# Kernel optimization log

Hardware: AMD Instinct MI355X
Metric: run time of the kernel (lower is better)

## Reference

```python
import jax, jax.numpy as jnp
import numpy as np

N_BATCH = 128   # C: number of PWL channels / generator batch
N_PTS = 32768   # N: samples per channel
K_PWL = 20      # breakpoints per piecewise-linear function
LATENT = 8
HID = 8
EPS = 1e-7


def _mlp(z, W1, b1, W2, b2):
    # torch mlp: Linear -> Tanh -> Linear -> Tanh
    h = jnp.tanh(z @ W1 + b1)
    return jnp.tanh(h @ W2 + b2)


def _normalize01(a):
    # per-row min/max normalization, a: [C, N]
    a = a - a.min(axis=1, keepdims=True)
    return a / a.max(axis=1, keepdims=True)


def _calibrate1d(x, xp, yp):
    # x: [N, C], xp/yp: [C, K]
    N, C = x.shape
    K = xp.shape[1]
    bp = jnp.concatenate([x[:, :, None], jnp.broadcast_to(xp[None], (N, C, K))], axis=2)  # [N,C,K+1]
    order = jnp.argsort(bp, axis=2)                       # [N,C,K+1]
    sorted_bp = jnp.take_along_axis(bp, order, axis=2)
    x_idx = jnp.argmin(order, axis=2)                     # rank of x among breakpoints
    cand = x_idx - 1
    start_idx = jnp.where(x_idx == 0, 1, jnp.where(x_idx == K, K - 2, cand))
    end_idx = jnp.where(start_idx == cand, start_idx + 2, start_idx + 1)
    start_x = jnp.take_along_axis(sorted_bp, start_idx[..., None], axis=2)[..., 0]
    end_x = jnp.take_along_axis(sorted_bp, end_idx[..., None], axis=2)[..., 0]
    start_idx2 = jnp.where(x_idx == 0, 0, jnp.where(x_idx == K, K - 2, cand))
    yp_e = jnp.broadcast_to(yp[None], (N, C, K))
    start_y = jnp.take_along_axis(yp_e, start_idx2[..., None], axis=2)[..., 0]
    end_y = jnp.take_along_axis(yp_e, (start_idx2 + 1)[..., None], axis=2)[..., 0]
    return start_y + (x - start_x) * (end_y - start_y) / (end_x - start_x + EPS)


def setup_inputs() -> dict:
    key = jax.random.key(0)
    ks = jax.random.split(key, 16)
    s = 0.5
    f32 = jnp.float32
    return {
        "zf": jax.random.normal(ks[0], (N_BATCH, LATENT), f32),
        "zx": jax.random.normal(ks[1], (N_BATCH, N_PTS, LATENT), f32),
        "ze": jax.random.normal(ks[2], (N_BATCH, N_PTS, LATENT), f32),
        "Wx1": jax.random.normal(ks[3], (LATENT, HID), f32) * s,
        "bx1": jax.random.normal(ks[4], (HID,), f32) * s,
        "Wx2": jax.random.normal(ks[5], (HID, 1), f32) * s,
        "bx2": jax.random.normal(ks[6], (1,), f32) * s,
        "We1": jax.random.normal(ks[7], (LATENT, HID), f32) * s,
        "be1": jax.random.normal(ks[8], (HID,), f32) * s,
        "We2": jax.random.normal(ks[9], (HID, 1), f32) * s,
        "be2": jax.random.normal(ks[10], (1,), f32) * s,
        "Wf1": jax.random.normal(ks[11], (LATENT, HID), f32) * s,
        "bf1": jax.random.normal(ks[12], (HID,), f32) * s,
        "Wf2": jax.random.normal(ks[13], (HID, K_PWL), f32) * s,
        "bf2": jax.random.normal(ks[14], (K_PWL,), f32) * s,
        "directions": jax.random.randint(ks[15], (N_BATCH,), 0, 2) > 0,
    }


def reference(zf, zx, ze, Wx1, bx1, Wx2, bx2, We1, be1, We2, be2, Wf1, bf1, Wf2, bf2, directions):
    # gen_f: random ascending/descending monotone PWL per channel
    pts = _mlp(zf, Wf1, bf1, Wf2, bf2)                        # [C, K]
    asc = jnp.sort(pts, axis=1)
    yp = jnp.where(directions[:, None], asc, asc[:, ::-1])    # [C, K]
    xp = jnp.broadcast_to(jnp.linspace(0.0, 1.0, K_PWL, dtype=pts.dtype)[None, :], yp.shape)
    # forward_x: cause variable, per-channel normalized to [0,1]
    x = _mlp(zx, Wx1, bx1, Wx2, bx2)[..., 0]                  # [C, N]
    x = _normalize01(x).T                                     # [N, C]
    # forward_e: standardized noise (global mean / unbiased std)
    e = _mlp(ze, We1, be1, We2, be2)[..., 0].T                # [N, C]
    e = (e - e.mean()) / e.std(ddof=1)
    # forward_y
    y = _calibrate1d(x, xp, yp) + 0.1 * e                     # [N, C]
    return y
```

## Files before the change

### kernel.cpp

```cpp
#include <hip/hip_runtime.h>

#define C_CH  128
#define NP    32768
#define K_PWL 20
#define LAT   8
#define HID   8
#define SLOTS 32
#define PTS   4

__device__ __forceinline__ float fast_tanh(float x) {
    float e = __expf(2.0f * x);
    return fmaf(-2.0f, __builtin_amdgcn_rcpf(e + 1.0f), 1.0f);
}

__device__ __forceinline__ unsigned fenc(float f) {
    unsigned u = __float_as_uint(f);
    return (u & 0x80000000u) ? ~u : (u | 0x80000000u);
}
__device__ __forceinline__ float fdec(unsigned e) {
    unsigned u = (e & 0x80000000u) ? (e ^ 0x80000000u) : ~e;
    return __uint_as_float(u);
}

__global__ void prep(const float* __restrict__ zf,
                     const float* __restrict__ Wf1, const float* __restrict__ bf1,
                     const float* __restrict__ Wf2, const float* __restrict__ bf2,
                     const unsigned char* __restrict__ dirs_raw,
                     float* __restrict__ ypw,
                     unsigned* cminE, unsigned* cmaxE, double* sums) {
    int t = threadIdx.x;
    if (t < C_CH) { cminE[t] = 0xFFFFFFFFu; cmaxE[t] = 0u; }
    if (t < 2 * SLOTS) sums[t] = 0.0;

    __shared__ int is_i32;
    if (t == 0) {
        const int* di = (const int*)dirs_raw;
        int ok = 1;
        for (int i = 0; i < 32; i++) { int v = di[i]; if (v != 0 && v != 1) ok = 0; }
        is_i32 = ok;
    }
    __syncthreads();
    if (t >= C_CH) return;
    int c = t;

    float z[LAT];
    #pragma unroll
    for (int l = 0; l < LAT; l++) z[l] = zf[c * LAT + l];
    float h[HID];
    #pragma unroll
    for (int j = 0; j < HID; j++) {
        float a = bf1[j];
        #pragma unroll
        for (int l = 0; l < LAT; l++) a = fmaf(z[l], Wf1[l * HID + j], a);
        h[j] = fast_tanh(a);
    }
    float p[K_PWL];
    #pragma unroll
    for (int k = 0; k < K_PWL; k++) {
        float a = bf2[k];
        #pragma unroll
        for (int j = 0; j < HID; j++) a = fmaf(h[j], Wf2[j * K_PWL + k], a);
        p[k] = fast_tanh(a);
    }
    for (int i = 1; i < K_PWL; i++) {
        float key = p[i];
        int j = i - 1;
        while (j >= 0 && p[j] > key) { p[j + 1] = p[j]; j--; }
        p[j + 1] = key;
    }
    int dir = is_i32 ? (((const int*)dirs_raw)[c] != 0) : (dirs_raw[c] != 0);
    for (int k = 0; k < K_PWL; k++)
        ypw[c * K_PWL + k] = dir ? p[k] : p[K_PWL - 1 - k];
}

__global__ __launch_bounds__(256)
void pass1(const float* __restrict__ zx, const float* __restrict__ ze,
           const float* __restrict__ Wx1, const float* __restrict__ bx1,
           const float* __restrict__ Wx2, const float* __restrict__ bx2,
           const float* __restrict__ We1, const float* __restrict__ be1,
           const float* __restrict__ We2, const float* __restrict__ be2,
           float* __restrict__ xraw, float* __restrict__ eraw,
           unsigned* __restrict__ cminE, unsigned* __restrict__ cmaxE,
           double* __restrict__ sums) {
    __shared__ float sw[162];
    int t = threadIdx.x;
    if (t < 64)       sw[t] = Wx1[t];
    else if (t < 72)  sw[t] = bx1[t - 64];
    else if (t < 80)  sw[t] = Wx2[t - 72];
    else if (t == 80) sw[80] = bx2[0];
    else if (t < 145) sw[t] = We1[t - 81];
    else if (t < 153) sw[t] = be1[t - 145];
    else if (t < 161) sw[t] = We2[t - 153];
    else if (t == 161) sw[161] = be2[0];
    __syncthreads();

    int c = blockIdx.y;
    int n0 = blockIdx.x * (256 * PTS) + t;
    size_t row = (size_t)c * NP;
    const float4* zx4 = (const float4*)(zx + row * LAT);
    const float4* ze4 = (const float4*)(ze + row * LAT);

    float4 ax[PTS][2], ae[PTS][2];
    #pragma unroll
    for (int k = 0; k < PTS; k++) {
        int n = n0 + k * 256;
        ax[k][0] = zx4[2 * n];  ax[k][1] = zx4[2 * n + 1];
        ae[k][0] = ze4[2 * n];  ae[k][1] = ze4[2 * n + 1];
    }

    float xv[PTS], ev[PTS];
    #pragma unroll
    for (int k = 0; k < PTS; k++) {
        float acc = sw[80];
        #pragma unroll
        for (int j = 0; j < HID; j++) {
            float hh = sw[64 + j];
            hh = fmaf(ax[k][0].x, sw[0 * 8 + j], hh);
            hh = fmaf(ax[k][0].y, sw[1 * 8 + j], hh);
            hh = fmaf(ax[k][0].z, sw[2 * 8 + j], hh);
            hh = fmaf(ax[k][0].w, sw[3 * 8 + j], hh);
            hh = fmaf(ax[k][1].x, sw[4 * 8 + j], hh);
            hh = fmaf(ax[k][1].y, sw[5 * 8 + j], hh);
            hh = fmaf(ax[k][1].z, sw[6 * 8 + j], hh);
            hh = fmaf(ax[k][1].w, sw[7 * 8 + j], hh);
            acc = fmaf(fast_tanh(hh), sw[72 + j], acc);
        }
        xv[k] = fast_tanh(acc);
    }
    #pragma unroll
    for (int k = 0; k < PTS; k++) {
        float acc = sw[161];
        #pragma unroll
        for (int j = 0; j < HID; j++) {
            float hh = sw[145 + j];
            hh = fmaf(ae[k][0].x, sw[81 + 0 * 8 + j], hh);
            hh = fmaf(ae[k][0].y, sw[81 + 1 * 8 + j], hh);
            hh = fmaf(ae[k][0].z, sw[81 + 2 * 8 + j], hh);
            hh = fmaf(ae[k][0].w, sw[81 + 3 * 8 + j], hh);
            hh = fmaf(ae[k][1].x, sw[81 + 4 * 8 + j], hh);
            hh = fmaf(ae[k][1].y, sw[81 + 5 * 8 + j], hh);
            hh = fmaf(ae[k][1].z, sw[81 + 6 * 8 + j], hh);
            hh = fmaf(ae[k][1].w, sw[81 + 7 * 8 + j], hh);
            acc = fmaf(fast_tanh(hh), sw[153 + j], acc);
        }
        ev[k] = fast_tanh(acc);
    }

    float mn = xv[0], mx = xv[0], s = 0.f, s2 = 0.f;
    #pragma unroll
    for (int k = 0; k < PTS; k++) {
        xraw[row + n0 + k * 256] = xv[k];
        eraw[row + n0 + k * 256] = ev[k];
        mn = fminf(mn, xv[k]); mx = fmaxf(mx, xv[k]);
        s += ev[k]; s2 += ev[k] * ev[k];
    }

    #pragma unroll
    for (int o = 32; o > 0; o >>= 1) {
        mn = fminf(mn, __shfl_down(mn, o));
        mx = fmaxf(mx, __shfl_down(mx, o));
        s += __shfl_down(s, o);
        s2 += __shfl_down(s2, o);
    }
    __shared__ float rmn[4], rmx[4], rs[4], rs2[4];
    int wave = t >> 6, lane = t & 63;
    if (lane == 0) { rmn[wave] = mn; rmx[wave] = mx; rs[wave] = s; rs2[wave] = s2; }
    __syncthreads();
    if (t == 0) {
        for (int w = 1; w < 4; w++) {
            mn = fminf(mn, rmn[w]); mx = fmaxf(mx, rmx[w]);
            s += rs[w]; s2 += rs2[w];
        }
        atomicMin(&cminE[c], fenc(mn));
        atomicMax(&cmaxE[c], fenc(mx));
        int slot = (blockIdx.x + blockIdx.y) & (SLOTS - 1);
        atomicAdd(&sums[2 * slot], (double)s);
        atomicAdd(&sums[2 * slot + 1], (double)s2);
    }
}

__global__ __launch_bounds__(256)
void pass2(const float* __restrict__ xraw, const float* __restrict__ eraw,
           const float* __restrict__ ypw,
           const unsigned* __restrict__ cminE, const unsigned* __restrict__ cmaxE,
           const double* __restrict__ sums,
           float* __restrict__ out) {
    __shared__ float ytile[C_CH * 33];
    __shared__ float syp[C_CH * K_PWL];
    __shared__ float smin[C_CH], sinv[C_CH];
    __shared__ float sstat[2];

    int t = threadIdx.x;
    for (int i = t; i < C_CH * K_PWL; i += 256) syp[i] = ypw[i];
    if (t < C_CH) {
        float mn = fdec(cminE[t]);
        float mx = fdec(cmaxE[t]);
        smin[t] = mn;
        sinv[t] = __builtin_amdgcn_rcpf(mx - mn);
    }
    if (t == 0) {
        double s = 0.0, s2 = 0.0;
        for (int i = 0; i < SLOTS; i++) { s += sums[2 * i]; s2 += sums[2 * i + 1]; }
        double M = (double)C_CH * NP;
        double mean = s / M;
        double var = (s2 - s * s / M) / (M - 1.0);
        sstat[0] = (float)mean;
        sstat[1] = (float)(0.1 / sqrt(var));
    }
    __syncthreads();

    const float INV_DENOM = 1.0f / (1.0f / 19.0f + 1e-7f);
    float mean = sstat[0], escale = sstat[1];
    int n0 = blockIdx.x * 32;

    #pragma unroll
    for (int i = 0; i < 16; i++) {
        int idx = i * 256 + t;
        int c = idx >> 5;
        int j = idx & 31;
        size_t g = (size_t)c * NP + (n0 + j);
        float x = xraw[g];
        float e = eraw[g];
        float xn = (x - smin[c]) * sinv[c];
        int seg = (int)floorf(xn * 19.0f);
        seg = max(0, min(18, seg));
        float y0 = syp[c * K_PWL + seg];
        float y1 = syp[c * K_PWL + seg + 1];
        float y = fmaf((xn - (float)seg * (1.0f / 19.0f)) * INV_DENOM, y1 - y0, y0);
        y = fmaf(e - mean, escale, y);
        ytile[c * 33 + j] = y;
    }
    __syncthreads();
    #pragma unroll
    for (int i = 0; i < 16; i++) {
        int idx = i * 256 + t;
        int j = idx >> 7;
        int c = idx & 127;
        out[(size_t)(n0 + j) * C_CH + c] = ytile[c * 33 + j];
    }
}

extern "C" void kernel_launch(void* const* d_in, const int* in_sizes, int n_in,
                              void* d_out, int out_size, void* d_ws, size_t ws_size,
                              hipStream_t stream) {
    const float* zf  = (const float*)d_in[0];
    const float* zx  = (const float*)d_in[1];
    const float* ze  = (const float*)d_in[2];
    const float* Wx1 = (const float*)d_in[3];
    const float* bx1 = (const float*)d_in[4];
    const float* Wx2 = (const float*)d_in[5];
    const float* bx2 = (const float*)d_in[6];
    const float* We1 = (const float*)d_in[7];
    const float* be1 = (const float*)d_in[8];
    const float* We2 = (const float*)d_in[9];
    const float* be2 = (const float*)d_in[10];
    const float* Wf1 = (const float*)d_in[11];
    const float* bf1 = (const float*)d_in[12];
    const float* Wf2 = (const float*)d_in[13];
    const float* bf2 = (const float*)d_in[14];
    const unsigned char* dirs = (const unsigned char*)d_in[15];

    float* xraw = (float*)d_ws;
    float* eraw = xraw + (size_t)C_CH * NP;
    float* ypw  = eraw + (size_t)C_CH * NP;
    unsigned* cminE = (unsigned*)(ypw + C_CH * K_PWL);
    unsigned* cmaxE = cminE + C_CH;
    double* sums = (double*)(cmaxE + C_CH);

    hipLaunchKernelGGL(prep, dim3(1), dim3(256), 0, stream,
                       zf, Wf1, bf1, Wf2, bf2, dirs, ypw, cminE, cmaxE, sums);
    hipLaunchKernelGGL(pass1, dim3(NP / (256 * PTS), C_CH), dim3(256), 0, stream,
                       zx, ze, Wx1, bx1, Wx2, bx2, We1, be1, We2, be2,
                       xraw, eraw, cminE, cmaxE, sums);
    hipLaunchKernelGGL(pass2, dim3(NP / 32), dim3(256), 0, stream,
                       xraw, eraw, ypw, cminE, cmaxE, sums, (float*)d_out);
}
```

Measured before the change: 344.1 us.

## Fuse prep, pass1 and pass2 into one cooperative kernel with grid syncs

Result: no change. 342.0 us (-0.6%).

```diff
diff --git a/kernel.cpp b/kernel.cpp
--- a/kernel.cpp
+++ b/kernel.cpp
@@ -1,4 +1,7 @@
 #include <hip/hip_runtime.h>
+#include <hip/hip_cooperative_groups.h>
+
+namespace cg = cooperative_groups;
 
 #define C_CH  128
 #define NP    32768
@@ -7,6 +10,8 @@
 #define HID   8
 #define SLOTS 32
 #define PTS   4
+#define NBLK  512
+#define TN    64
 
 __device__ __forceinline__ float fast_tanh(float x) {
     float e = __expf(2.0f * x);
@@ -20,6 +25,239 @@
 __device__ __forceinline__ float fdec(unsigned e) {
     unsigned u = (e & 0x80000000u) ? (e ^ 0x80000000u) : ~e;
     return __uint_as_float(u);
+}
+
+__device__ __forceinline__ float mlp_eval(const float* W, float4 r0, float4 r1) {
+    float acc = W[80];
+    #pragma unroll
+    for (int j = 0; j < HID; j++) {
+        float hh = W[64 + j];
+        hh = fmaf(r0.x, W[0 * 8 + j], hh);
+        hh = fmaf(r0.y, W[1 * 8 + j], hh);
+        hh = fmaf(r0.z, W[2 * 8 + j], hh);
+        hh = fmaf(r0.w, W[3 * 8 + j], hh);
+        hh = fmaf(r1.x, W[4 * 8 + j], hh);
+        hh = fmaf(r1.y, W[5 * 8 + j], hh);
+        hh = fmaf(r1.z, W[6 * 8 + j], hh);
+        hh = fmaf(r1.w, W[7 * 8 + j], hh);
+        acc = fmaf(fast_tanh(hh), W[72 + j], acc);
+    }
+    return fast_tanh(acc);
+}
+
+__global__ __launch_bounds__(256, 2)
+void fused(const float* __restrict__ zf, const float* __restrict__ zx,
+           const float* __restrict__ ze,
+           const float* __restrict__ Wx1, const float* __restrict__ bx1,
+           const float* __restrict__ Wx2, const float* __restrict__ bx2,
+           const float* __restrict__ We1, const float* __restrict__ be1,
+           const float* __restrict__ We2, const float* __restrict__ be2,
+           const float* __restrict__ Wf1, const float* __restrict__ bf1,
+           const float* __restrict__ Wf2, const float* __restrict__ bf2,
+           const unsigned char* __restrict__ dirs_raw,
+           float* __restrict__ out,
+           double* __restrict__ psum,
+           float* __restrict__ pmin,
+           float* __restrict__ pmax,
+           float* __restrict__ gmm,
+           float* __restrict__ gstat) {
+    __shared__ float sx[C_CH * (TN + 1)];
+    __shared__ float se[C_CH * TN];
+    __shared__ float syp[C_CH * K_PWL];
+    __shared__ float sw[162];
+    __shared__ float smin[C_CH], sinv[C_CH];
+    __shared__ float sstat2[2];
+    __shared__ float rf[8];
+    __shared__ double rsd[8];
+    __shared__ int is_i32;
+
+    int t = threadIdx.x;
+    int b = blockIdx.x;
+    int w = t >> 6, lane = t & 63;
+
+    if (t < 64)        sw[t] = Wx1[t];
+    else if (t < 72)   sw[t] = bx1[t - 64];
+    else if (t < 80)   sw[t] = Wx2[t - 72];
+    else if (t == 80)  sw[80] = bx2[0];
+    else if (t < 145)  sw[t] = We1[t - 81];
+    else if (t < 153)  sw[t] = be1[t - 145];
+    else if (t < 161)  sw[t] = We2[t - 153];
+    else if (t == 161) sw[161] = be2[0];
+    if (t == 192) {
+        const int* di = (const int*)dirs_raw;
+        int ok = 1;
+        for (int i = 0; i < 32; i++) { int v = di[i]; if (v != 0 && v != 1) ok = 0; }
+        is_i32 = ok;
+    }
+    __syncthreads();
+
+    int n0 = b * TN;
+    const float4* zx4 = (const float4*)zx + ((size_t)w * NP + n0 + lane) * 2;
+    const float4* ze4 = (const float4*)ze + ((size_t)w * NP + n0 + lane) * 2;
+    const size_t STEP = (size_t)4 * NP * 2;
+
+    float ssum = 0.f, ss2 = 0.f;
+    float4 A0 = zx4[0], A1 = zx4[1], AE0 = ze4[0], AE1 = ze4[1];
+    float4 B0 = zx4[STEP], B1 = zx4[STEP + 1], BE0 = ze4[STEP], BE1 = ze4[STEP + 1];
+    #pragma unroll 2
+    for (int i = 0; i < 32; i++) {
+        float4 C0, C1, CE0, CE1;
+        if (i + 2 < 32) {
+            size_t o = (size_t)(i + 2) * STEP;
+            C0 = zx4[o]; C1 = zx4[o + 1]; CE0 = ze4[o]; CE1 = ze4[o + 1];
+        } else { C0 = B0; C1 = B1; CE0 = BE0; CE1 = BE1; }
+        float xv = mlp_eval(sw, A0, A1);
+        float ev = mlp_eval(sw + 81, AE0, AE1);
+        int idx = i * 256 + t;
+        sx[idx + (idx >> 6)] = xv;
+        se[idx] = ev;
+        ssum += ev;
+        ss2 = fmaf(ev, ev, ss2);
+        A0 = B0; A1 = B1; AE0 = BE0; AE1 = BE1;
+        B0 = C0; B1 = C1; BE0 = CE0; BE1 = CE1;
+    }
+
+    #pragma unroll
+    for (int o = 32; o > 0; o >>= 1) {
+        ssum += __shfl_down(ssum, o);
+        ss2  += __shfl_down(ss2, o);
+    }
+    if (lane == 0) { rf[w] = ssum; rf[4 + w] = ss2; }
+    __syncthreads();
+
+    if (t < C_CH) {
+        float mn = 3.0e38f, mx = -3.0e38f;
+        int base = t * (TN + 1);
+        #pragma unroll 8
+        for (int j = 0; j < TN; j++) {
+            float v = sx[base + j];
+            mn = fminf(mn, v); mx = fmaxf(mx, v);
+        }
+        pmin[b * C_CH + t] = mn;
+        pmax[b * C_CH + t] = mx;
+        if (t == 0) {
+            double S  = (double)rf[0] + (double)rf[1] + (double)rf[2] + (double)rf[3];
+            double S2 = (double)rf[4] + (double)rf[5] + (double)rf[6] + (double)rf[7];
+            psum[2 * b] = S; psum[2 * b + 1] = S2;
+        }
+    } else {
+        int c = t - 128;
+        float z[LAT];
+        #pragma unroll
+        for (int l = 0; l < LAT; l++) z[l] = zf[c * LAT + l];
+        float h[HID];
+        #pragma unroll
+        for (int j = 0; j < HID; j++) {
+            float a = bf1[j];
+            #pragma unroll
+            for (int l = 0; l < LAT; l++) a = fmaf(z[l], Wf1[l * HID + j], a);
+            h[j] = fast_tanh(a);
+        }
+        float p[K_PWL];
+        #pragma unroll
+        for (int k = 0; k < K_PWL; k++) {
+            float a = bf2[k];
+            #pragma unroll
+            for (int j = 0; j < HID; j++) a = fmaf(h[j], Wf2[j * K_PWL + k], a);
+            p[k] = fast_tanh(a);
+        }
+        #pragma unroll
+        for (int ph = 0; ph < K_PWL; ph++) {
+            #pragma unroll
+            for (int k = (ph & 1); k + 1 < K_PWL; k += 2) {
+                float lo = fminf(p[k], p[k + 1]);
+                float hi = fmaxf(p[k], p[k + 1]);
+                p[k] = lo; p[k + 1] = hi;
+            }
+        }
+        int dir = is_i32 ? (((const int*)dirs_raw)[c] != 0) : (dirs_raw[c] != 0);
+        #pragma unroll
+        for (int k = 0; k < K_PWL; k++)
+            syp[c * K_PWL + k] = dir ? p[k] : p[K_PWL - 1 - k];
+    }
+
+    __threadfence();
+    cg::grid_group grid = cg::this_grid();
+    grid.sync();
+
+    if (b < C_CH) {
+        const volatile float* vmin = pmin;
+        const volatile float* vmax = pmax;
+        float mn = fminf(vmin[(size_t)t * C_CH + b], vmin[(size_t)(t + 256) * C_CH + b]);
+        float mx = fmaxf(vmax[(size_t)t * C_CH + b], vmax[(size_t)(t + 256) * C_CH + b]);
+        #pragma unroll
+        for (int o = 32; o > 0; o >>= 1) {
+            mn = fminf(mn, __shfl_down(mn, o));
+            mx = fmaxf(mx, __shfl_down(mx, o));
+        }
+        if (lane == 0) { rf[w] = mn; rf[4 + w] = mx; }
+        __syncthreads();
+        if (t == 0) {
+            mn = fminf(fminf(rf[0], rf[1]), fminf(rf[2], rf[3]));
+            mx = fmaxf(fmaxf(rf[4], rf[5]), fmaxf(rf[6], rf[7]));
+            gmm[b] = mn; gmm[C_CH + b] = mx;
+        }
+    } else if (b == C_CH) {
+        const volatile double* vs = psum;
+        double S  = vs[2 * t]     + vs[2 * (t + 256)];
+        double S2 = vs[2 * t + 1] + vs[2 * (t + 256) + 1];
+        #pragma unroll
+        for (int o = 32; o > 0; o >>= 1) {
+            S  += __shfl_down(S, o);
+            S2 += __shfl_down(S2, o);
+        }
+        if (lane == 0) { rsd[w] = S; rsd[4 + w] = S2; }
+        __syncthreads();
+        if (t == 0) {
+            S  = rsd[0] + rsd[1] + rsd[2] + rsd[3];
+            S2 = rsd[4] + rsd[5] + rsd[6] + rsd[7];
+            double M = (double)C_CH * NP;
+            double mean = S / M;
+            double var = (S2 - S * S / M) / (M - 1.0);
+            gstat[0] = (float)mean;
+            gstat[1] = (float)(0.1 / sqrt(var));
+        }
+    }
+    __threadfence();
+    grid.sync();
+
+    if (t < C_CH) {
+        const volatile float* g = gmm;
+        float mn = g[t], mx = g[C_CH + t];
+        smin[t] = mn;
+        sinv[t] = __builtin_amdgcn_rcpf(mx - mn);
+    }
+    if (t == 0) {
+        const volatile float* gs = gstat;
+        sstat2[0] = gs[0]; sstat2[1] = gs[1];
+    }
+    __syncthreads();
+
+    const float INV_DENOM = 1.0f / (1.0f / 19.0f + 1e-7f);
+    float mean = sstat2[0], escale = sstat2[1];
+    #pragma unroll 4
+    for (int i = 0; i < 32; i++) {
+        int idx = i * 256 + t;
+        int c = idx >> 6;
+        float x = sx[idx + c];
+        float e = se[idx];
+        float xn = (x - smin[c]) * sinv[c];
+        int seg = (int)floorf(xn * 19.0f);
+        seg = max(0, min(18, seg));
+        float y0 = syp[c * K_PWL + seg];
+        float y1 = syp[c * K_PWL + seg + 1];
+        float y = fmaf((xn - (float)seg * (1.0f / 19.0f)) * INV_DENOM, y1 - y0, y0);
+        y = fmaf(e - mean, escale, y);
+        sx[idx + c] = y;
+    }
+    __syncthreads();
+    #pragma unroll 4
+    for (int ii = 0; ii < 32; ii++) {
+        int idx2 = ii * 256 + t;
+        int c = idx2 & 127;
+        int j = idx2 >> 7;
+        out[(size_t)(n0 + j) * C_CH + c] = sx[c * (TN + 1) + j];
+    }
 }
 
 __global__ void prep(const float* __restrict__ zf,
@@ -110,41 +348,9 @@
 
     float xv[PTS], ev[PTS];
     #pragma unroll
-    for (int k = 0; k < PTS; k++) {
-        float acc = sw[80];
-        #pragma unroll
-        for (int j = 0; j < HID; j++) {
-            float hh = sw[64 + j];
-            hh = fmaf(ax[k][0].x, sw[0 * 8 + j], hh);
-            hh = fmaf(ax[k][0].y, sw[1 * 8 + j], hh);
-            hh = fmaf(ax[k][0].z, sw[2 * 8 + j], hh);
-            hh = fmaf(ax[k][0].w, sw[3 * 8 + j], hh);
-            hh = fmaf(ax[k][1].x, sw[4 * 8 + j], hh);
-            hh = fmaf(ax[k][1].y, sw[5 * 8 + j], hh);
-            hh = fmaf(ax[k][1].z, sw[6 * 8 + j], hh);
-            hh = fmaf(ax[k][1].w, sw[7 * 8 + j], hh);
-            acc = fmaf(fast_tanh(hh), sw[72 + j], acc);
-        }
-        xv[k] = fast_tanh(acc);
-    }
-    #pragma unroll
-    for (int k = 0; k < PTS; k++) {
-        float acc = sw[161];
-        #pragma unroll
-        for (int j = 0; j < HID; j++) {
-            float hh = sw[145 + j];
-            hh = fmaf(ae[k][0].x, sw[81 + 0 * 8 + j], hh);
-            hh = fmaf(ae[k][0].y, sw[81 + 1 * 8 + j], hh);
-            hh = fmaf(ae[k][0].z, sw[81 + 2 * 8 + j], hh);
-            hh = fmaf(ae[k][0].w, sw[81 + 3 * 8 + j], hh);
-            hh = fmaf(ae[k][1].x, sw[81 + 4 * 8 + j], hh);
-            hh = fmaf(ae[k][1].y, sw[81 + 5 * 8 + j], hh);
-            hh = fmaf(ae[k][1].z, sw[81 + 6 * 8 + j], hh);
-            hh = fmaf(ae[k][1].w, sw[81 + 7 * 8 + j], hh);
-            acc = fmaf(fast_tanh(hh), sw[153 + j], acc);
-        }
-        ev[k] = fast_tanh(acc);
-    }
+    for (int k = 0; k < PTS; k++) xv[k] = mlp_eval(sw, ax[k][0], ax[k][1]);
+    #pragma unroll
+    for (int k = 0; k < PTS; k++) ev[k] = mlp_eval(sw + 81, ae[k][0], ae[k][1]);
 
     float mn = xv[0], mx = xv[0], s = 0.f, s2 = 0.f;
     #pragma unroll
@@ -259,6 +465,38 @@
     const float* Wf2 = (const float*)d_in[13];
     const float* bf2 = (const float*)d_in[14];
     const unsigned char* dirs = (const unsigned char*)d_in[15];
+    float* outp = (float*)d_out;
+
+    static int mode = -1;
+    if (mode < 0) {
+        int dev = 0, coop = 0, nb = 0;
+        hipGetDevice(&dev);
+        hipDeviceGetAttribute(&coop, hipDeviceAttributeCooperativeLaunch, dev);
+        hipError_t oe = hipOccupancyMaxActiveBlocksPerMultiprocessor(
+            &nb, reinterpret_cast<const void*>(fused), 256, 0);
+        mode = (coop && oe == hipSuccess && nb >= 2) ? 1 : 0;
+    }
+
+    if (mode == 1) {
+        double* psum  = (double*)d_ws;
+        float*  pmin  = (float*)(psum + 2 * NBLK);
+        float*  pmax  = pmin + NBLK * C_CH;
+        float*  gmm   = pmax + NBLK * C_CH;
+        float*  gstat = gmm + 2 * C_CH;
+        void* args[] = {
+            (void*)&zf,  (void*)&zx,  (void*)&ze,
+            (void*)&Wx1, (void*)&bx1, (void*)&Wx2, (void*)&bx2,
+            (void*)&We1, (void*)&be1, (void*)&We2, (void*)&be2,
+            (void*)&Wf1, (void*)&bf1, (void*)&Wf2, (void*)&bf2,
+            (void*)&dirs, (void*)&outp,
+            (void*)&psum, (void*)&pmin, (void*)&pmax, (void*)&gmm, (void*)&gstat
+        };
+        hipError_t le = hipLaunchCooperativeKernel(
+            reinterpret_cast<const void*>(fused), dim3(NBLK), dim3(256),
+            args, 0, stream);
+        if (le == hipSuccess) return;
+        mode = 0;
+    }
 
     float* xraw = (float*)d_ws;
     float* eraw = xraw + (size_t)C_CH * NP;
@@ -273,5 +511,5 @@
                        zx, ze, Wx1, bx1, Wx2, bx2, We1, be1, We2, be2,
                        xraw, eraw, cminE, cmaxE, sums);
     hipLaunchKernelGGL(pass2, dim3(NP / 32), dim3(256), 0, stream,
-                       xraw, eraw, ypw, cminE, cmaxE, sums, (float*)d_out);
-}
+                       xraw, eraw, ypw, cminE, cmaxE, sums, outp);
+}
```

## Store pass1 intermediates in pass2 tile layout and halve points per thread

Applied to the files above, without the earlier changes.

After: 416.6 us. 1.21x slower.

```diff
diff --git a/kernel.cpp b/kernel.cpp
--- a/kernel.cpp
+++ b/kernel.cpp
@@ -6,7 +6,7 @@
 #define LAT   8
 #define HID   8
 #define SLOTS 32
-#define PTS   4
+#define P1PTS 2
 
 __device__ __forceinline__ float fast_tanh(float x) {
     float e = __expf(2.0f * x);
@@ -20,6 +20,24 @@
 __device__ __forceinline__ float fdec(unsigned e) {
     unsigned u = (e & 0x80000000u) ? (e ^ 0x80000000u) : ~e;
     return __uint_as_float(u);
+}
+
+__device__ __forceinline__ float mlp_eval(const float* W, float4 r0, float4 r1) {
+    float acc = W[80];
+    #pragma unroll
+    for (int j = 0; j < HID; j++) {
+        float hh = W[64 + j];
+        hh = fmaf(r0.x, W[0 * 8 + j], hh);
+        hh = fmaf(r0.y, W[1 * 8 + j], hh);
+        hh = fmaf(r0.z, W[2 * 8 + j], hh);
+        hh = fmaf(r0.w, W[3 * 8 + j], hh);
+        hh = fmaf(r1.x, W[4 * 8 + j], hh);
+        hh = fmaf(r1.y, W[5 * 8 + j], hh);
+        hh = fmaf(r1.z, W[6 * 8 + j], hh);
+        hh = fmaf(r1.w, W[7 * 8 + j], hh);
+        acc = fmaf(fast_tanh(hh), W[72 + j], acc);
+    }
+    return fast_tanh(acc);
 }
 
 __global__ void prep(const float* __restrict__ zf,
@@ -73,15 +91,15 @@
         ypw[c * K_PWL + k] = dir ? p[k] : p[K_PWL - 1 - k];
 }
 
-__global__ __launch_bounds__(256)
-void pass1(const float* __restrict__ zx, const float* __restrict__ ze,
-           const float* __restrict__ Wx1, const float* __restrict__ bx1,
-           const float* __restrict__ Wx2, const float* __restrict__ bx2,
-           const float* __restrict__ We1, const float* __restrict__ be1,
-           const float* __restrict__ We2, const float* __restrict__ be2,
-           float* __restrict__ xraw, float* __restrict__ eraw,
-           unsigned* __restrict__ cminE, unsigned* __restrict__ cmaxE,
-           double* __restrict__ sums) {
+__global__ __launch_bounds__(256, 8)
+void pass1t(const float* __restrict__ zx, const float* __restrict__ ze,
+            const float* __restrict__ Wx1, const float* __restrict__ bx1,
+            const float* __restrict__ Wx2, const float* __restrict__ bx2,
+            const float* __restrict__ We1, const float* __restrict__ be1,
+            const float* __restrict__ We2, const float* __restrict__ be2,
+            float* __restrict__ xtile, float* __restrict__ etile,
+            unsigned* __restrict__ cminE, unsigned* __restrict__ cmaxE,
+            double* __restrict__ sums) {
     __shared__ float sw[162];
     int t = threadIdx.x;
     if (t < 64)       sw[t] = Wx1[t];
@@ -95,62 +113,33 @@
     __syncthreads();
 
     int c = blockIdx.y;
-    int n0 = blockIdx.x * (256 * PTS) + t;
+    int n0 = blockIdx.x * (256 * P1PTS) + t;
     size_t row = (size_t)c * NP;
     const float4* zx4 = (const float4*)(zx + row * LAT);
     const float4* ze4 = (const float4*)(ze + row * LAT);
 
-    float4 ax[PTS][2], ae[PTS][2];
-    #pragma unroll
-    for (int k = 0; k < PTS; k++) {
+    float4 ax[P1PTS][2], ae[P1PTS][2];
+    #pragma unroll
+    for (int k = 0; k < P1PTS; k++) {
         int n = n0 + k * 256;
         ax[k][0] = zx4[2 * n];  ax[k][1] = zx4[2 * n + 1];
         ae[k][0] = ze4[2 * n];  ae[k][1] = ze4[2 * n + 1];
     }
 
-    float xv[PTS], ev[PTS];
-    #pragma unroll
-    for (int k = 0; k < PTS; k++) {
-        float acc = sw[80];
-        #pragma unroll
-        for (int j = 0; j < HID; j++) {
-            float hh = sw[64 + j];
-            hh = fmaf(ax[k][0].x, sw[0 * 8 + j], hh);
-            hh = fmaf(ax[k][0].y, sw[1 * 8 + j], hh);
-            hh = fmaf(ax[k][0].z, sw[2 * 8 + j], hh);
-            hh = fmaf(ax[k][0].w, sw[3 * 8 + j], hh);
-            hh = fmaf(ax[k][1].x, sw[4 * 8 + j], hh);
-            hh = fmaf(ax[k][1].y, sw[5 * 8 + j], hh);
-            hh = fmaf(ax[k][1].z, sw[6 * 8 + j], hh);
-            hh = fmaf(ax[k][1].w, sw[7 * 8 + j], hh);
-            acc = fmaf(fast_tanh(hh), sw[72 + j], acc);
-        }
-        xv[k] = fast_tanh(acc);
-    }
-    #pragma unroll
-    for (int k = 0; k < PTS; k++) {
-        float acc = sw[161];
-        #pragma unroll
-        for (int j = 0; j < HID; j++) {
-            float hh = sw[145 + j];
-            hh = fmaf(ae[k][0].x, sw[81 + 0 * 8 + j], hh);
-            hh = fmaf(ae[k][0].y, sw[81 + 1 * 8 + j], hh);
-            hh = fmaf(ae[k][0].z, sw[81 + 2 * 8 + j], hh);
-            hh = fmaf(ae[k][0].w, sw[81 + 3 * 8 + j], hh);
-            hh = fmaf(ae[k][1].x, sw[81 + 4 * 8 + j], hh);
-            hh = fmaf(ae[k][1].y, sw[81 + 5 * 8 + j], hh);
-            hh = fmaf(ae[k][1].z, sw[81 + 6 * 8 + j], hh);
-            hh = fmaf(ae[k][1].w, sw[81 + 7 * 8 + j], hh);
-            acc = fmaf(fast_tanh(hh), sw[153 + j], acc);
-        }
-        ev[k] = fast_tanh(acc);
-    }
+    float xv[P1PTS], ev[P1PTS];
+    #pragma unroll
+    for (int k = 0; k < P1PTS; k++) xv[k] = mlp_eval(sw, ax[k][0], ax[k][1]);
+    #pragma unroll
+    for (int k = 0; k < P1PTS; k++) ev[k] = mlp_eval(sw + 81, ae[k][0], ae[k][1]);
 
     float mn = xv[0], mx = xv[0], s = 0.f, s2 = 0.f;
-    #pragma unroll
-    for (int k = 0; k < PTS; k++) {
-        xraw[row + n0 + k * 256] = xv[k];
-        eraw[row + n0 + k * 256] = ev[k];
+    int cbase = c * 32;
+    #pragma unroll
+    for (int k = 0; k < P1PTS; k++) {
+        int n = n0 + k * 256;
+        int addr = (n >> 5) * (C_CH * 32) + cbase + (n & 31);
+        xtile[addr] = xv[k];
+        etile[addr] = ev[k];
         mn = fminf(mn, xv[k]); mx = fmaxf(mx, xv[k]);
         s += ev[k]; s2 += ev[k] * ev[k];
     }
@@ -180,11 +169,11 @@
 }
 
 __global__ __launch_bounds__(256)
-void pass2(const float* __restrict__ xraw, const float* __restrict__ eraw,
-           const float* __restrict__ ypw,
-           const unsigned* __restrict__ cminE, const unsigned* __restrict__ cmaxE,
-           const double* __restrict__ sums,
-           float* __restrict__ out) {
+void pass2t(const float* __restrict__ xtile, const float* __restrict__ etile,
+            const float* __restrict__ ypw,
+            const unsigned* __restrict__ cminE, const unsigned* __restrict__ cmaxE,
+            const double* __restrict__ sums,
+            float* __restrict__ out) {
     __shared__ float ytile[C_CH * 33];
     __shared__ float syp[C_CH * K_PWL];
     __shared__ float smin[C_CH], sinv[C_CH];
@@ -211,6 +200,7 @@
 
     const float INV_DENOM = 1.0f / (1.0f / 19.0f + 1e-7f);
     float mean = sstat[0], escale = sstat[1];
+    size_t tbase = (size_t)blockIdx.x * (C_CH * 32);
     int n0 = blockIdx.x * 32;
 
     #pragma unroll
@@ -218,9 +208,8 @@
         int idx = i * 256 + t;
         int c = idx >> 5;
         int j = idx & 31;
-        size_t g = (size_t)c * NP + (n0 + j);
-        float x = xraw[g];
-        float e = eraw[g];
+        float x = xtile[tbase + idx];
+        float e = etile[tbase + idx];
         float xn = (x - smin[c]) * sinv[c];
         int seg = (int)floorf(xn * 19.0f);
         seg = max(0, min(18, seg));
@@ -260,18 +249,18 @@
     const float* bf2 = (const float*)d_in[14];
     const unsigned char* dirs = (const unsigned char*)d_in[15];
 
-    float* xraw = (float*)d_ws;
-    float* eraw = xraw + (size_t)C_CH * NP;
-    float* ypw  = eraw + (size_t)C_CH * NP;
+    float* xtile = (float*)d_ws;
+    float* etile = xtile + (size_t)C_CH * NP;
+    float* ypw   = etile + (size_t)C_CH * NP;
     unsigned* cminE = (unsigned*)(ypw + C_CH * K_PWL);
     unsigned* cmaxE = cminE + C_CH;
     double* sums = (double*)(cmaxE + C_CH);
 
     hipLaunchKernelGGL(prep, dim3(1), dim3(256), 0, stream,
                        zf, Wf1, bf1, Wf2, bf2, dirs, ypw, cminE, cmaxE, sums);
-    hipLaunchKernelGGL(pass1, dim3(NP / (256 * PTS), C_CH), dim3(256), 0, stream,
+    hipLaunchKernelGGL(pass1t, dim3(NP / (256 * P1PTS), C_CH), dim3(256), 0, stream,
                        zx, ze, Wx1, bx1, Wx2, bx2, We1, be1, We2, be2,
-                       xraw, eraw, cminE, cmaxE, sums);
-    hipLaunchKernelGGL(pass2, dim3(NP / 32), dim3(256), 0, stream,
-                       xraw, eraw, ypw, cminE, cmaxE, sums, (float*)d_out);
-}
+                       xtile, etile, cminE, cmaxE, sums);
+    hipLaunchKernelGGL(pass2t, dim3(NP / 32), dim3(256), 0, stream,
+                       xtile, etile, ypw, cminE, cmaxE, sums, (float*)d_out);
+}
```
